# Optimization experiments

Hardware: AMD Instinct MI355X
Metric: run time of the kernel (lower is better)

The kernel has to match this reference:

```python
import jax, jax.numpy as jnp
import numpy as np

INIT_STDEV = 0.01

def setup_inputs() -> dict:
    key = jax.random.key(0)
    k1, k2, k3 = jax.random.split(key, 3)
    B, S, D = 8, 4096, 768
    x = jax.random.normal(k1, (B, S, D), dtype=jnp.float32)
    att_v = jax.random.normal(k2, (D,), dtype=jnp.float32) * INIT_STDEV
    att_W = jax.random.normal(k3, (D, D), dtype=jnp.float32) * INIT_STDEV
    return {"x": x, "att_v": att_v, "att_W": att_W}

def reference(x, att_v, att_W):
    # y = x @ W : [B,S,D]; scores = tanh(y) . v over D : [B,S]
    y = jnp.tanh(jnp.einsum('bsd,de->bse', x, att_W))
    scores = jnp.einsum('bsd,d->bs', y, att_v)
    weights = jax.nn.softmax(scores, axis=-1)            # softmax over sequence
    out = jnp.einsum('bs,bsd->bd', weights, x)           # attsum pool
    return out.astype(jnp.float32)
```

## Files before the change

kernel.cpp:

```cpp
#include <hip/hip_runtime.h>
#include <hip/hip_bf16.h>

constexpr int Bb = 8;
constexpr int Ss = 4096;
constexpr int Dd = 768;
constexpr int Mm = Bb * Ss;

constexpr int BM = 64;
constexpr int KCH = 4;

typedef __bf16 bf16x8 __attribute__((ext_vector_type(8)));
typedef __bf16 bf16x4 __attribute__((ext_vector_type(4)));
typedef float f32x4 __attribute__((ext_vector_type(4)));

__device__ __forceinline__ float fast_tanh(float x) {
    return 1.f - 2.f / (__expf(2.f * x) + 1.f);
}

__global__ __launch_bounds__(256) void convW(const float* __restrict__ W,
                                             __bf16* __restrict__ Wt) {
    __shared__ float tile[32][33];
    const int tx = threadIdx.x & 31;
    const int ty = threadIdx.x >> 5;
    const int kb = blockIdx.x * 32;
    const int nb = blockIdx.y * 32;
#pragma unroll
    for (int i = 0; i < 32; i += 8)
        tile[ty + i][tx] = W[(size_t)(kb + ty + i) * Dd + nb + tx];
    __syncthreads();
#pragma unroll
    for (int i = 0; i < 32; i += 8)
        Wt[(size_t)(nb + ty + i) * Dd + kb + tx] = (__bf16)tile[tx][ty + i];
}

__global__ __launch_bounds__(512, 2) void scores_gemm(
    const float* __restrict__ x, const __bf16* __restrict__ Wt,
    const float* __restrict__ v, float* __restrict__ scores) {
    __shared__ __bf16 As[24 * 4 * 64 * 8];
    __shared__ float sc_sh[8][BM];

    const int t = threadIdx.x;
    const int mb = blockIdx.x;
    const int lane = t & 63;
    const int w = t >> 6;
    const int quad = lane >> 4;
    const int lid = lane & 15;

    const float* xb = x + (size_t)mb * BM * Dd;

    float4 sreg[6];
    auto load_chunk = [&](int c) {
#pragma unroll
        for (int j = 0; j < 6; ++j) {
            const int idx = j * 512 + t;
            const int row = idx / 48;
            const int c4 = idx - row * 48;
            sreg[j] = *(const float4*)(xb + (size_t)row * Dd + c * 192 + c4 * 4);
        }
    };
    auto store_chunk = [&](int c) {
#pragma unroll
        for (int j = 0; j < 6; ++j) {
            const int idx = j * 512 + t;
            const int row = idx / 48;
            const int c4 = idx - row * 48;
            const int k0 = c * 192 + c4 * 4;
            const int kb = k0 >> 5;
            const int qd = (k0 >> 3) & 3;
            const int j0 = k0 & 7;
            const int tm = row >> 4;
            const int ld = row & 15;
            bf16x4 p;
            p[0] = (__bf16)sreg[j].x; p[1] = (__bf16)sreg[j].y;
            p[2] = (__bf16)sreg[j].z; p[3] = (__bf16)sreg[j].w;
            *(bf16x4*)(&As[(((kb * 4 + tm) * 64) + qd * 16 + ld) * 8 + j0]) = p;
        }
    };

    const __bf16* wp[6];
#pragma unroll
    for (int nt = 0; nt < 6; ++nt)
        wp[nt] = Wt + (size_t)(w * 96 + nt * 16 + lid) * Dd + quad * 8;

    f32x4 acc[4][6];
#pragma unroll
    for (int tm = 0; tm < 4; ++tm)
#pragma unroll
        for (int nt = 0; nt < 6; ++nt) acc[tm][nt] = (f32x4){0.f, 0.f, 0.f, 0.f};

    load_chunk(0);
    store_chunk(0);

    bf16x8 bcur[6], bnxt[6];
#pragma unroll
    for (int nt = 0; nt < 6; ++nt) bcur[nt] = *(const bf16x8*)(wp[nt]);

    bf16x8 afc[4], afn[4];

    for (int c = 0; c < KCH; ++c) {
        __syncthreads();
        if (c < KCH - 1) load_chunk(c + 1);
        {
            const int kb = c * 6;
#pragma unroll
            for (int tm = 0; tm < 4; ++tm)
                afc[tm] = *(const bf16x8*)(&As[((kb * 4 + tm) * 64 + lane) * 8]);
        }
#pragma unroll
        for (int kk = 0; kk < 6; ++kk) {
            const int kb = c * 6 + kk;
            if (kb + 1 < 24) {
#pragma unroll
                for (int nt = 0; nt < 6; ++nt)
                    bnxt[nt] = *(const bf16x8*)(wp[nt] + (kb + 1) * 32);
            }
            if (kk < 5) {
#pragma unroll
                for (int tm = 0; tm < 4; ++tm)
                    afn[tm] = *(const bf16x8*)(&As[(((kb + 1) * 4 + tm) * 64 + lane) * 8]);
            }
#pragma unroll
            for (int tm = 0; tm < 4; ++tm)
#pragma unroll
                for (int nt = 0; nt < 6; ++nt)
                    acc[tm][nt] = __builtin_amdgcn_mfma_f32_16x16x32_bf16(afc[tm], bcur[nt], acc[tm][nt], 0, 0, 0);
#pragma unroll
            for (int tm = 0; tm < 4; ++tm) afc[tm] = afn[tm];
#pragma unroll
            for (int nt = 0; nt < 6; ++nt) bcur[nt] = bnxt[nt];
        }
        if (c < KCH - 1) store_chunk(c + 1);
    }

    float vv[6];
#pragma unroll
    for (int nt = 0; nt < 6; ++nt) vv[nt] = v[w * 96 + nt * 16 + lid];

#pragma unroll
    for (int tm = 0; tm < 4; ++tm)
#pragma unroll
        for (int r = 0; r < 4; ++r) {
            float s = 0.f;
#pragma unroll
            for (int nt = 0; nt < 6; ++nt) s += vv[nt] * fast_tanh(acc[tm][nt][r]);
            s += __shfl_xor(s, 1);
            s += __shfl_xor(s, 2);
            s += __shfl_xor(s, 4);
            s += __shfl_xor(s, 8);
            if (lid == 0) sc_sh[w][tm * 16 + quad * 4 + r] = s;
        }
    __syncthreads();
    if (t < BM) {
        float s = 0.f;
#pragma unroll
        for (int ww = 0; ww < 8; ++ww) s += sc_sh[ww][t];
        scores[mb * BM + t] = s;
    }
}

__global__ __launch_bounds__(256) void softmax_k(const float* __restrict__ scores,
                                                 float* __restrict__ weights) {
    const int b = blockIdx.x;
    const int t = threadIdx.x;
    const float* s = scores + (size_t)b * Ss;
    float* wgt = weights + (size_t)b * Ss;
    __shared__ float red[256];

    float mx = -1e30f;
    for (int i = t; i < Ss; i += 256) mx = fmaxf(mx, s[i]);
    red[t] = mx;
    __syncthreads();
    for (int o = 128; o > 0; o >>= 1) {
        if (t < o) red[t] = fmaxf(red[t], red[t + o]);
        __syncthreads();
    }
    mx = red[0];
    __syncthreads();
    float sum = 0.f;
    for (int i = t; i < Ss; i += 256) {
        const float e = __expf(s[i] - mx);
        wgt[i] = e;
        sum += e;
    }
    red[t] = sum;
    __syncthreads();
    for (int o = 128; o > 0; o >>= 1) {
        if (t < o) red[t] += red[t + o];
        __syncthreads();
    }
    const float inv = 1.f / red[0];
    for (int i = t; i < Ss; i += 256) wgt[i] *= inv;
}

__global__ __launch_bounds__(192) void pool_k(const float* __restrict__ x,
                                              const float* __restrict__ weights,
                                              float* __restrict__ out) {
    const int b = blockIdx.y;
    const int sc = blockIdx.x;
    const int t = threadIdx.x;
    const int s0 = sc * 32;
    float4 acc = make_float4(0.f, 0.f, 0.f, 0.f);
#pragma unroll 8
    for (int i = 0; i < 32; ++i) {
        const int s = s0 + i;
        const float ww = weights[(size_t)b * Ss + s];
        const float4 xv = *(const float4*)(x + ((size_t)b * Ss + s) * Dd + t * 4);
        acc.x += ww * xv.x;
        acc.y += ww * xv.y;
        acc.z += ww * xv.z;
        acc.w += ww * xv.w;
    }
    float* o = out + (size_t)b * Dd + t * 4;
    atomicAdd(o + 0, acc.x);
    atomicAdd(o + 1, acc.y);
    atomicAdd(o + 2, acc.z);
    atomicAdd(o + 3, acc.w);
}

extern "C" void kernel_launch(void* const* d_in, const int* in_sizes, int n_in,
                              void* d_out, int out_size, void* d_ws, size_t ws_size,
                              hipStream_t stream) {
    (void)in_sizes; (void)n_in; (void)ws_size;
    const float* x = (const float*)d_in[0];
    const float* v = (const float*)d_in[1];
    const float* W = (const float*)d_in[2];

    char* ws = (char*)d_ws;
    __bf16* Wt = (__bf16*)ws;
    float* scores = (float*)(ws + 1179648);
    float* weights = (float*)(ws + 1179648 + 131072);

    hipMemsetAsync(d_out, 0, (size_t)out_size * sizeof(float), stream);

    convW<<<dim3(Dd / 32, Dd / 32), 256, 0, stream>>>(W, Wt);
    scores_gemm<<<dim3(Mm / BM), 512, 0, stream>>>(x, Wt, v, scores);
    softmax_k<<<dim3(Bb), 256, 0, stream>>>(scores, weights);
    pool_k<<<dim3(128, Bb), 192, 0, stream>>>(x, weights, (float*)d_out);
}
```

Measured before the change: 271.8 us.

## Retile scores GEMM to 128x128 with direct-to-LDS loads and two-stage pooling

Replaces the per-row-block GEMM, which held the full K extent of A in LDS as bf16, with a 128x128 output tile over a 2D grid. Each K step loads fp32 x and bf16 W straight into LDS with global_load_lds, converts A to bf16 at fragment load time, and combines per-N-tile score partials with atomicAdd into a zeroed scores buffer. Pooling is split into a partial-sum kernel and a reduction kernel, replacing the float atomics into the output. The GEMM is single-buffered with two barriers per K step and no overlap, and x is now read six times (once per N tile) instead of once.

```diff
diff --git a/kernel.cpp b/kernel.cpp
--- a/kernel.cpp
+++ b/kernel.cpp
@@ -6,15 +6,17 @@
 constexpr int Dd = 768;
 constexpr int Mm = Bb * Ss;
 
-constexpr int BM = 64;
-constexpr int KCH = 4;
-
 typedef __bf16 bf16x8 __attribute__((ext_vector_type(8)));
-typedef __bf16 bf16x4 __attribute__((ext_vector_type(4)));
 typedef float f32x4 __attribute__((ext_vector_type(4)));
 
 __device__ __forceinline__ float fast_tanh(float x) {
     return 1.f - 2.f / (__expf(2.f * x) + 1.f);
+}
+
+__device__ __forceinline__ void load_lds16(const void* g, void* l) {
+    __builtin_amdgcn_global_load_lds(
+        (const __attribute__((address_space(1))) unsigned int*)g,
+        (__attribute__((address_space(3))) unsigned int*)l, 16, 0, 0);
 }
 
 __global__ __launch_bounds__(256) void convW(const float* __restrict__ W,
@@ -33,108 +35,82 @@
         Wt[(size_t)(nb + ty + i) * Dd + kb + tx] = (__bf16)tile[tx][ty + i];
 }
 
-__global__ __launch_bounds__(512, 2) void scores_gemm(
+__global__ __launch_bounds__(256) void scores_gemm(
     const float* __restrict__ x, const __bf16* __restrict__ Wt,
     const float* __restrict__ v, float* __restrict__ scores) {
-    __shared__ __bf16 As[24 * 4 * 64 * 8];
-    __shared__ float sc_sh[8][BM];
+    __shared__ float As[128 * 32];
+    __shared__ __bf16 Bs[128 * 32];
+    __shared__ float ssc[2][128];
 
     const int t = threadIdx.x;
-    const int mb = blockIdx.x;
+    const int nb = blockIdx.x;
+    const int mb = blockIdx.y;
     const int lane = t & 63;
-    const int w = t >> 6;
+    const int wave = t >> 6;
+    const int wm = wave >> 1;
+    const int wn = wave & 1;
     const int quad = lane >> 4;
     const int lid = lane & 15;
 
-    const float* xb = x + (size_t)mb * BM * Dd;
-
-    float4 sreg[6];
-    auto load_chunk = [&](int c) {
-#pragma unroll
-        for (int j = 0; j < 6; ++j) {
-            const int idx = j * 512 + t;
-            const int row = idx / 48;
-            const int c4 = idx - row * 48;
-            sreg[j] = *(const float4*)(xb + (size_t)row * Dd + c * 192 + c4 * 4);
+    const float* ag[4]; float* al[4];
+#pragma unroll
+    for (int j = 0; j < 4; ++j) {
+        const int flat = j * 4096 + t * 16;
+        const int row = flat >> 7;
+        const int colb = flat & 127;
+        ag[j] = x + (size_t)(mb * 128 + row) * Dd + (colb >> 2);
+        al[j] = &As[flat >> 2];
+    }
+    const __bf16* bg[2]; __bf16* bl[2];
+#pragma unroll
+    for (int j = 0; j < 2; ++j) {
+        const int flat = j * 4096 + t * 16;
+        const int row = flat >> 6;
+        const int colb = flat & 63;
+        bg[j] = Wt + (size_t)(nb * 128 + row) * Dd + (colb >> 1);
+        bl[j] = &Bs[flat >> 1];
+    }
+
+    f32x4 acc[4][4];
+#pragma unroll
+    for (int i = 0; i < 4; ++i)
+#pragma unroll
+        for (int j = 0; j < 4; ++j) acc[i][j] = (f32x4){0.f, 0.f, 0.f, 0.f};
+
+    for (int kb = 0; kb < 24; ++kb) {
+#pragma unroll
+        for (int j = 0; j < 4; ++j) load_lds16(ag[j] + kb * 32, al[j]);
+#pragma unroll
+        for (int j = 0; j < 2; ++j) load_lds16(bg[j] + kb * 32, bl[j]);
+        __syncthreads();
+
+        bf16x8 af[4], bfr[4];
+#pragma unroll
+        for (int tm = 0; tm < 4; ++tm) {
+            const float* ap = &As[(wm * 64 + tm * 16 + lid) * 32 + quad * 8];
+            const float4 lo = *(const float4*)ap;
+            const float4 hi = *(const float4*)(ap + 4);
+            bf16x8 a;
+            a[0] = (__bf16)lo.x; a[1] = (__bf16)lo.y; a[2] = (__bf16)lo.z; a[3] = (__bf16)lo.w;
+            a[4] = (__bf16)hi.x; a[5] = (__bf16)hi.y; a[6] = (__bf16)hi.z; a[7] = (__bf16)hi.w;
+            af[tm] = a;
         }
-    };
-    auto store_chunk = [&](int c) {
-#pragma unroll
-        for (int j = 0; j < 6; ++j) {
-            const int idx = j * 512 + t;
-            const int row = idx / 48;
-            const int c4 = idx - row * 48;
-            const int k0 = c * 192 + c4 * 4;
-            const int kb = k0 >> 5;
-            const int qd = (k0 >> 3) & 3;
-            const int j0 = k0 & 7;
-            const int tm = row >> 4;
-            const int ld = row & 15;
-            bf16x4 p;
-            p[0] = (__bf16)sreg[j].x; p[1] = (__bf16)sreg[j].y;
-            p[2] = (__bf16)sreg[j].z; p[3] = (__bf16)sreg[j].w;
-            *(bf16x4*)(&As[(((kb * 4 + tm) * 64) + qd * 16 + ld) * 8 + j0]) = p;
-        }
-    };
-
-    const __bf16* wp[6];
-#pragma unroll
-    for (int nt = 0; nt < 6; ++nt)
-        wp[nt] = Wt + (size_t)(w * 96 + nt * 16 + lid) * Dd + quad * 8;
-
-    f32x4 acc[4][6];
-#pragma unroll
-    for (int tm = 0; tm < 4; ++tm)
-#pragma unroll
-        for (int nt = 0; nt < 6; ++nt) acc[tm][nt] = (f32x4){0.f, 0.f, 0.f, 0.f};
-
-    load_chunk(0);
-    store_chunk(0);
-
-    bf16x8 bcur[6], bnxt[6];
-#pragma unroll
-    for (int nt = 0; nt < 6; ++nt) bcur[nt] = *(const bf16x8*)(wp[nt]);
-
-    bf16x8 afc[4], afn[4];
-
-    for (int c = 0; c < KCH; ++c) {
-        __syncthreads();
-        if (c < KCH - 1) load_chunk(c + 1);
-        {
-            const int kb = c * 6;
-#pragma unroll
-            for (int tm = 0; tm < 4; ++tm)
-                afc[tm] = *(const bf16x8*)(&As[((kb * 4 + tm) * 64 + lane) * 8]);
-        }
-#pragma unroll
-        for (int kk = 0; kk < 6; ++kk) {
-            const int kb = c * 6 + kk;
-            if (kb + 1 < 24) {
-#pragma unroll
-                for (int nt = 0; nt < 6; ++nt)
-                    bnxt[nt] = *(const bf16x8*)(wp[nt] + (kb + 1) * 32);
-            }
-            if (kk < 5) {
-#pragma unroll
-                for (int tm = 0; tm < 4; ++tm)
-                    afn[tm] = *(const bf16x8*)(&As[(((kb + 1) * 4 + tm) * 64 + lane) * 8]);
-            }
-#pragma unroll
-            for (int tm = 0; tm < 4; ++tm)
-#pragma unroll
-                for (int nt = 0; nt < 6; ++nt)
-                    acc[tm][nt] = __builtin_amdgcn_mfma_f32_16x16x32_bf16(afc[tm], bcur[nt], acc[tm][nt], 0, 0, 0);
-#pragma unroll
-            for (int tm = 0; tm < 4; ++tm) afc[tm] = afn[tm];
-#pragma unroll
-            for (int nt = 0; nt < 6; ++nt) bcur[nt] = bnxt[nt];
-        }
-        if (c < KCH - 1) store_chunk(c + 1);
-    }
-
-    float vv[6];
-#pragma unroll
-    for (int nt = 0; nt < 6; ++nt) vv[nt] = v[w * 96 + nt * 16 + lid];
+#pragma unroll
+        for (int tn = 0; tn < 4; ++tn)
+            bfr[tn] = *(const bf16x8*)&Bs[(wn * 64 + tn * 16 + lid) * 32 + quad * 8];
+
+#pragma unroll
+        for (int tm = 0; tm < 4; ++tm)
+#pragma unroll
+            for (int tn = 0; tn < 4; ++tn)
+                acc[tm][tn] = __builtin_amdgcn_mfma_f32_16x16x32_bf16(af[tm], bfr[tn], acc[tm][tn], 0, 0, 0);
+        __syncthreads();
+    }
+
+    float vv[4];
+#pragma unroll
+    for (int tn = 0; tn < 4; ++tn)
+        vv[tn] = v[nb * 128 + wn * 64 + tn * 16 + lid];
 
 #pragma unroll
     for (int tm = 0; tm < 4; ++tm)
@@ -142,20 +118,16 @@
         for (int r = 0; r < 4; ++r) {
             float s = 0.f;
 #pragma unroll
-            for (int nt = 0; nt < 6; ++nt) s += vv[nt] * fast_tanh(acc[tm][nt][r]);
+            for (int tn = 0; tn < 4; ++tn) s += vv[tn] * fast_tanh(acc[tm][tn][r]);
             s += __shfl_xor(s, 1);
             s += __shfl_xor(s, 2);
             s += __shfl_xor(s, 4);
             s += __shfl_xor(s, 8);
-            if (lid == 0) sc_sh[w][tm * 16 + quad * 4 + r] = s;
+            if (lid == 0) ssc[wn][wm * 64 + tm * 16 + quad * 4 + r] = s;
         }
     __syncthreads();
-    if (t < BM) {
-        float s = 0.f;
-#pragma unroll
-        for (int ww = 0; ww < 8; ++ww) s += sc_sh[ww][t];
-        scores[mb * BM + t] = s;
-    }
+    if (t < 128)
+        atomicAdd(&scores[mb * 128 + t], ssc[0][t] + ssc[1][t]);
 }
 
 __global__ __launch_bounds__(256) void softmax_k(const float* __restrict__ scores,
@@ -192,35 +164,41 @@
     for (int i = t; i < Ss; i += 256) wgt[i] *= inv;
 }
 
-__global__ __launch_bounds__(192) void pool_k(const float* __restrict__ x,
-                                              const float* __restrict__ weights,
-                                              float* __restrict__ out) {
+__global__ __launch_bounds__(192) void pool1(const float* __restrict__ x,
+                                             const float* __restrict__ weights,
+                                             float* __restrict__ partial) {
     const int b = blockIdx.y;
-    const int sc = blockIdx.x;
+    const int c = blockIdx.x;
     const int t = threadIdx.x;
-    const int s0 = sc * 32;
+    const float* base = x + ((size_t)b * Ss + c * 64) * Dd;
+    const float* wrow = weights + (size_t)b * Ss + c * 64;
     float4 acc = make_float4(0.f, 0.f, 0.f, 0.f);
 #pragma unroll 8
-    for (int i = 0; i < 32; ++i) {
-        const int s = s0 + i;
-        const float ww = weights[(size_t)b * Ss + s];
-        const float4 xv = *(const float4*)(x + ((size_t)b * Ss + s) * Dd + t * 4);
+    for (int i = 0; i < 64; ++i) {
+        const float ww = wrow[i];
+        const float4 xv = *(const float4*)(base + (size_t)i * Dd + t * 4);
         acc.x += ww * xv.x;
         acc.y += ww * xv.y;
         acc.z += ww * xv.z;
         acc.w += ww * xv.w;
     }
-    float* o = out + (size_t)b * Dd + t * 4;
-    atomicAdd(o + 0, acc.x);
-    atomicAdd(o + 1, acc.y);
-    atomicAdd(o + 2, acc.z);
-    atomicAdd(o + 3, acc.w);
+    *(float4*)(partial + ((size_t)(b * 64 + c)) * Dd + t * 4) = acc;
+}
+
+__global__ __launch_bounds__(768) void pool2(const float* __restrict__ partial,
+                                             float* __restrict__ out) {
+    const int b = blockIdx.x;
+    const int d = threadIdx.x;
+    float s = 0.f;
+#pragma unroll 8
+    for (int c = 0; c < 64; ++c) s += partial[((size_t)(b * 64 + c)) * Dd + d];
+    out[(size_t)b * Dd + d] = s;
 }
 
 extern "C" void kernel_launch(void* const* d_in, const int* in_sizes, int n_in,
                               void* d_out, int out_size, void* d_ws, size_t ws_size,
                               hipStream_t stream) {
-    (void)in_sizes; (void)n_in; (void)ws_size;
+    (void)in_sizes; (void)n_in; (void)ws_size; (void)out_size;
     const float* x = (const float*)d_in[0];
     const float* v = (const float*)d_in[1];
     const float* W = (const float*)d_in[2];
@@ -229,11 +207,13 @@
     __bf16* Wt = (__bf16*)ws;
     float* scores = (float*)(ws + 1179648);
     float* weights = (float*)(ws + 1179648 + 131072);
-
-    hipMemsetAsync(d_out, 0, (size_t)out_size * sizeof(float), stream);
+    float* partial = (float*)(ws + 1179648 + 262144);
+
+    hipMemsetAsync(scores, 0, Mm * sizeof(float), stream);
 
     convW<<<dim3(Dd / 32, Dd / 32), 256, 0, stream>>>(W, Wt);
-    scores_gemm<<<dim3(Mm / BM), 512, 0, stream>>>(x, Wt, v, scores);
+    scores_gemm<<<dim3(6, Mm / 128), 256, 0, stream>>>(x, Wt, v, scores);
     softmax_k<<<dim3(Bb), 256, 0, stream>>>(scores, weights);
-    pool_k<<<dim3(128, Bb), 192, 0, stream>>>(x, weights, (float*)d_out);
-}
+    pool1<<<dim3(64, Bb), 192, 0, stream>>>(x, weights, partial);
+    pool2<<<dim3(Bb), 768, 0, stream>>>(partial, (float*)d_out);
+}
```

Result: slower. 378.8 us (+39.4%).
